# Kernel optimization log

Measured on AMD Instinct MI355X. Metric: run time of the kernel, lower is better.

The kernel has to match this reference:

```python
import jax, jax.numpy as jnp
import numpy as np

N, E, D_IN, D_H, D_OUT, W = 100000, 1600000, 128, 128, 128, 3
HTC_W, TEMP = 0.01, 1.0  # curvature c = 1.0


def _project(x):
    n = jnp.maximum(jnp.linalg.norm(x, axis=-1, keepdims=True), 1e-12)
    return x * jnp.minimum((1.0 - 1e-5) / n, 1.0)


def _artanh(x):
    x = jnp.clip(x, -1.0 + 1e-6, 1.0 - 1e-6)
    return 0.5 * (jnp.log1p(x) - jnp.log1p(-x))


def _expmap0(v):
    n = jnp.maximum(jnp.linalg.norm(v, axis=-1, keepdims=True), 1e-12)
    return _project(jnp.tanh(n) * v / n)


def _logmap0(y):
    y = _project(y)
    n = jnp.maximum(jnp.linalg.norm(y, axis=-1, keepdims=True), 1e-12)
    return _artanh(n) * y / n


def setup_inputs() -> dict:
    key = jax.random.key(0)
    ks = jax.random.split(key, 24)
    x = jax.random.normal(ks[0], (N, D_IN), dtype=jnp.float32)
    edge_index = jax.random.randint(ks[1], (2, E), 0, N)
    t = jax.random.uniform(ks[2], (E,), dtype=jnp.float32)
    prev_hyp = _project(jax.random.normal(ks[3], (N, D_OUT), dtype=jnp.float32) * 0.05)
    lengths = jax.random.randint(ks[4], (N,), 0, W + 1)
    valid_mask = jnp.arange(W)[None, :] < lengths[:, None]  # front-filled deque
    hist_hyp = _project(jax.random.normal(ks[5], (N, W, D_OUT), dtype=jnp.float32) * 0.05)
    hist_hyp = hist_hyp * valid_mask[..., None].astype(jnp.float32)  # padded slots are zero

    def lin(k, dout, din):
        return jax.random.normal(k, (dout, din), dtype=jnp.float32) / np.sqrt(din)

    params = dict(
        w_time=jax.random.normal(ks[6], (D_IN,), dtype=jnp.float32),
        b_time=jnp.zeros((D_IN,), jnp.float32),
        W0_l=lin(ks[7], D_H, D_IN), b0_l=jnp.zeros((D_H,), jnp.float32), W0_r=lin(ks[8], D_H, D_IN),
        W1_l=lin(ks[9], D_OUT, D_H), b1_l=jnp.zeros((D_OUT,), jnp.float32), W1_r=lin(ks[10], D_OUT, D_H),
        W_ih=lin(ks[11], 3 * D_OUT, D_OUT), W_hh=lin(ks[12], 3 * D_OUT, D_OUT),
        b_ih=jnp.zeros((3 * D_OUT,), jnp.float32), b_hh=jnp.zeros((3 * D_OUT,), jnp.float32),
        Wq=lin(ks[13], D_OUT, D_OUT), Wk=lin(ks[14], D_OUT, D_OUT), Wv=lin(ks[15], D_OUT, D_OUT),
    )
    return dict(x=x, edge_index=edge_index, t=t, prev_hyp=prev_hyp,
                hist_hyp=hist_hyp, valid_mask=valid_mask, **params)


def reference(x, edge_index, t, prev_hyp, hist_hyp, valid_mask,
              w_time, b_time, W0_l, b0_l, W0_r, W1_l, b1_l, W1_r,
              W_ih, W_hh, b_ih, b_hh, Wq, Wk, Wv):
    n = x.shape[0]
    src, dst = edge_index[0], edge_index[1]
    ones_e = jnp.ones_like(t)
    # per-node mean event time over incident edges (src and dst both count)
    nt = jax.ops.segment_sum(t, src, n) + jax.ops.segment_sum(t, dst, n)
    cnt = jax.ops.segment_sum(ones_e, src, n) + jax.ops.segment_sum(ones_e, dst, n)
    node_time = nt / jnp.maximum(cnt, 1.0)
    x = x + jnp.cos(node_time[:, None] * w_time[None, :] + b_time[None, :])
    # SAGEConv (mean aggr over incoming edges): out = W_l @ mean_j x_j + b + W_r @ x_i
    deg = jnp.maximum(jax.ops.segment_sum(ones_e, dst, n), 1.0)[:, None]
    agg0 = jax.ops.segment_sum(x[src], dst, n) / deg
    h = jax.nn.relu(agg0 @ W0_l.T + b0_l + x @ W0_r.T)
    agg1 = jax.ops.segment_sum(h[src], dst, n) / deg
    h_now = agg1 @ W1_l.T + b1_l + h @ W1_r.T  # tangent-space current embedding

    prev_tan = _logmap0(prev_hyp)
    # ragged history attention (padded + masked)
    hist_tan = _logmap0(hist_hyp)                       # [N, W, D]
    q = h_now @ Wq.T                                    # [N, D]
    k = hist_tan @ Wk.T                                 # [N, W, D]
    v = hist_tan @ Wv.T
    score = jnp.einsum('nwd,nd->nw', k, q) / (np.sqrt(D_OUT) * max(TEMP, 1e-6))
    has_hist = valid_mask.any(axis=-1, keepdims=True)
    score = jnp.where(valid_mask, score, -jnp.inf)
    score = jnp.where(has_hist, score, 0.0)
    alpha = jax.nn.softmax(score, axis=-1)
    alpha = jnp.where(has_hist, alpha, 0.0)
    ctx = jnp.einsum('nw,nwd->nd', alpha, v)

    # GRUCell(input=h_now, hidden=prev_tan + ctx)
    hidden = prev_tan + ctx
    gi = h_now @ W_ih.T + b_ih
    gh = hidden @ W_hh.T + b_hh
    i_r, i_z, i_n = jnp.split(gi, 3, axis=-1)
    h_r, h_z, h_n = jnp.split(gh, 3, axis=-1)
    r = jax.nn.sigmoid(i_r + h_r)
    z = jax.nn.sigmoid(i_z + h_z)
    nn_ = jnp.tanh(i_n + r * h_n)
    h_tan = (1.0 - z) * nn_ + z * hidden
    h_hyp = _expmap0(h_tan)

    # hyperbolic temporal consistency aux loss (c = 1)
    x_sq = jnp.sum(h_hyp * h_hyp, axis=-1)
    y_sq = jnp.sum(prev_hyp * prev_hyp, axis=-1)
    diff_sq = jnp.sum((h_hyp - prev_hyp) ** 2, axis=-1)
    denom = jnp.maximum((1.0 - x_sq) * (1.0 - y_sq), 1e-8)
    zarg = jnp.maximum(1.0 + 2.0 * diff_sq / denom, 1.0 + 1e-6)
    dist = jnp.arccosh(zarg)
    valid_prev = (jnp.sum(jnp.abs(prev_hyp), axis=-1) > 0).astype(dist.dtype)
    aux = HTC_W * jnp.sum(dist * valid_prev) / jnp.maximum(jnp.sum(valid_prev), 1.0)
    aux = jnp.where(jnp.any(valid_prev > 0), aux, 0.0)
    return h_hyp, aux
```

## Files before the change

kernel.cpp:

```cpp
#include <hip/hip_runtime.h>
#include <math.h>


typedef _Float16 f16x8 __attribute__((ext_vector_type(8)));
typedef _Float16 f16x4 __attribute__((ext_vector_type(4)));
typedef _Float16 f16x2 __attribute__((ext_vector_type(2)));
typedef float f32x4 __attribute__((ext_vector_type(4)));

__device__ __forceinline__ float wsum(float v) {
#pragma unroll
  for (int off = 1; off < 64; off <<= 1) v += __shfl_xor(v, off, 64);
  return v;
}

__device__ __forceinline__ void fsplit(float x, _Float16& h, _Float16& l) {
  h = (_Float16)x;
  l = (_Float16)(x - (float)h);
}

__device__ __forceinline__ float logmap_scale(float nrm2) {
  float n0 = fmaxf(sqrtf(nrm2), 1e-12f);
  float sp = fminf((1.0f - 1e-5f) / n0, 1.0f);
  float np = fmaxf(n0 * sp, 1e-12f);
  float a  = fminf(np, 1.0f - 1e-6f);
  float at = 0.5f * (log1pf(a) - log1pf(-a));
  return sp * at / np;
}

__global__ void k_edge(const int* __restrict__ ei, const float* __restrict__ t,
                       unsigned long long* __restrict__ packed, int E) {
  int e = blockIdx.x * 256 + threadIdx.x;
  if (e >= E) return;
  int s = ei[e], d = ei[E + e];
  unsigned long long tf =
      (unsigned long long)__float2uint_rn(t[e] * 16777216.0f);
  unsigned long long encs = tf | (1ULL << 40);
  atomicAdd(&packed[s], encs);
  atomicAdd(&packed[d], encs | (1ULL << 52));
}

__global__ void k_scan1(const unsigned long long* __restrict__ packed,
                        int* __restrict__ rowptr, int* __restrict__ bsum, int N) {
  __shared__ int s[256];
  int t = threadIdx.x;
  int base = blockIdx.x * 1024 + t * 4;
  int v[4]; int loc = 0;
#pragma unroll
  for (int j = 0; j < 4; ++j) {
    int i = base + j;
    v[j] = (i < N) ? (int)(packed[i] >> 52) : 0;
    loc += v[j];
  }
  s[t] = loc; __syncthreads();
  for (int off = 1; off < 256; off <<= 1) {
    int x = (t >= off) ? s[t - off] : 0; __syncthreads();
    s[t] += x; __syncthreads();
  }
  int run = s[t] - loc;
#pragma unroll
  for (int j = 0; j < 4; ++j) { int i = base + j; if (i < N) rowptr[i] = run; run += v[j]; }
  if (t == 255) bsum[blockIdx.x] = s[255];
}

__global__ void k_scan2(const int* __restrict__ bsum, int* __restrict__ boff, int nb) {
  __shared__ int s[128];
  int t = threadIdx.x;
  int v = (t < nb) ? bsum[t] : 0;
  s[t] = v; __syncthreads();
  for (int off = 1; off < 128; off <<= 1) {
    int x = (t >= off) ? s[t - off] : 0; __syncthreads();
    s[t] += x; __syncthreads();
  }
  boff[t] = s[t] - v;
}

__global__ void k_scan3(int* __restrict__ rowptr, const int* __restrict__ boff, int N, int E) {
  int i = blockIdx.x * 256 + threadIdx.x;
  if (i < N) rowptr[i] += boff[i >> 10];
  if (i == 0) rowptr[N] = E;
}

__global__ void k_scatter(const int* __restrict__ ei, const int* __restrict__ rowptr,
                          int* __restrict__ cursor, int* __restrict__ eidx, int E) {
  int e = blockIdx.x * 256 + threadIdx.x;
  if (e >= E) return;
  int s = ei[e], d = ei[E + e];
  int p = rowptr[d] + atomicAdd(&cursor[d], 1);
  eidx[p] = s;
}

__global__ void k_time(const float* __restrict__ x,
                       const unsigned long long* __restrict__ packed,
                       const float* __restrict__ wt,
                       const float* __restrict__ bt, float* __restrict__ outF,
                       _Float16* __restrict__ outH, _Float16* __restrict__ outL, int N) {
  int id = blockIdx.x * 256 + threadIdx.x;
  if (id >= N * 32) return;
  int n = id >> 5, q = id & 31;
  unsigned long long p = packed[n];
  float tsum = (float)(p & 0xFFFFFFFFFFULL) * 5.9604644775390625e-8f;
  int c = (int)((p >> 40) & 0xFFF);
  float tm = tsum / fmaxf((float)c, 1.0f);
  float4 xv = ((const float4*)x)[id];
  float4 wv = ((const float4*)wt)[q];
  float4 bv = ((const float4*)bt)[q];
  float o[4];
  o[0] = xv.x + cosf(tm * wv.x + bv.x);
  o[1] = xv.y + cosf(tm * wv.y + bv.y);
  o[2] = xv.z + cosf(tm * wv.z + bv.z);
  o[3] = xv.w + cosf(tm * wv.w + bv.w);
  ((float4*)outF)[id] = make_float4(o[0], o[1], o[2], o[3]);
  f16x4 vh, vl;
#pragma unroll
  for (int j = 0; j < 4; ++j) { _Float16 h, l; fsplit(o[j], h, l); vh[j] = h; vl[j] = l; }
  *(f16x4*)&outH[(size_t)id * 4] = vh;
  *(f16x4*)&outL[(size_t)id * 4] = vl;
}

__global__ void k_agg(const float* __restrict__ X, const int* __restrict__ rowptr,
                      const int* __restrict__ eidx, _Float16* __restrict__ outH,
                      _Float16* __restrict__ outL, int N) {
  int wid = threadIdx.x >> 6, lane = threadIdx.x & 63;
  int n = blockIdx.x * 4 + wid;
  if (n >= N) return;
  int s0 = rowptr[n], s1 = rowptr[n + 1];
  float ax = 0.f, ay = 0.f;
  for (int e = s0; e < s1; ++e) {
    int s = eidx[e];
    float2 v = ((const float2*)X)[(size_t)s * 64 + lane];
    ax += v.x; ay += v.y;
  }
  float sc = 1.0f / fmaxf((float)(s1 - s0), 1.0f);
  _Float16 hx, lx, hy, ly;
  fsplit(ax * sc, hx, lx); fsplit(ay * sc, hy, ly);
  f16x2 vh = {hx, hy}, vl = {lx, ly};
  *(f16x2*)&outH[(size_t)n * 128 + lane * 2] = vh;
  *(f16x2*)&outL[(size_t)n * 128 + lane * 2] = vl;
}

__global__ void k_prep(const float* __restrict__ W0l, const float* __restrict__ W0r,
                       const float* __restrict__ W1l, const float* __restrict__ W1r,
                       const float* __restrict__ Wv,  const float* __restrict__ Wih,
                       const float* __restrict__ Whh, const float* __restrict__ bih,
                       const float* __restrict__ bhh,
                       _Float16* __restrict__ W0H, _Float16* __restrict__ W0L,
                       _Float16* __restrict__ W1H, _Float16* __restrict__ W1L,
                       _Float16* __restrict__ WvH, _Float16* __restrict__ WvL,
                       _Float16* __restrict__ WzH, _Float16* __restrict__ WzL,
                       float* __restrict__ bz) {
  int id = blockIdx.x * 256 + threadIdx.x;
  if (id < 32768) {
    int c = id >> 8, k = id & 255;
    float v0 = (k < 128) ? W0l[c * 128 + k] : W0r[c * 128 + (k - 128)];
    float v1 = (k < 128) ? W1l[c * 128 + k] : W1r[c * 128 + (k - 128)];
    fsplit(v0, W0H[id], W0L[id]);
    fsplit(v1, W1H[id], W1L[id]);
  }
  if (id < 16384) {
    fsplit(Wv[id], WvH[id], WvL[id]);
  }
  if (id < 131072) {
    int c = id >> 8, k = id & 255;
    float v;
    if (c < 256)      v = (k < 128) ? Wih[c * 128 + k] : Whh[c * 128 + (k - 128)];
    else if (c < 384) v = (k < 128) ? Wih[c * 128 + k] : 0.f;
    else              v = (k < 128) ? 0.f : Whh[(c - 128) * 128 + (k - 128)];
    fsplit(v, WzH[id], WzL[id]);
  }
  if (id < 512) {
    float v;
    if (id < 256)      v = bih[id] + bhh[id];
    else if (id < 384) v = bih[id];
    else               v = bhh[id - 128];
    bz[id] = v;
  }
}

__global__ void k_ct(const float* __restrict__ Wk, const float* __restrict__ Wq,
                     _Float16* __restrict__ CtH, _Float16* __restrict__ CtL) {
  int id = blockIdx.x * 256 + threadIdx.x;
  if (id >= 16384) return;
  int c = id >> 7, k = id & 127;
  float s = 0.f;
  for (int j = 0; j < 128; ++j) s += Wk[j * 128 + c] * Wq[j * 128 + k];
  fsplit(s, CtH[id], CtL[id]);
}

__global__ __launch_bounds__(256)
void k_mm(const _Float16* __restrict__ A1H, const _Float16* __restrict__ A1L,
          const _Float16* __restrict__ A2H, const _Float16* __restrict__ A2L,
          const _Float16* __restrict__ WH,  const _Float16* __restrict__ WL,
          const float* __restrict__ bias,   const float* __restrict__ addb,
          float* __restrict__ outF, _Float16* __restrict__ outH,
          _Float16* __restrict__ outL,
          int Nrows, int Ktot, int Ctot, int relu) {
  __shared__ _Float16 sA[2][128][64];
  __shared__ _Float16 sW[2][128][64];
  const int tid = threadIdx.x;
  const int lane = tid & 63;
  const int wv = tid >> 6;
  const int wr = wv >> 1, wc = wv & 1;
  const int laneR = lane & 15, laneG = lane >> 4;
  const int n0 = blockIdx.x * 128;
  const int c0 = blockIdx.y * 128;

  f32x4 acc[4][4];
#pragma unroll
  for (int mi = 0; mi < 4; ++mi)
#pragma unroll
    for (int ni = 0; ni < 4; ++ni)
#pragma unroll
      for (int j = 0; j < 4; ++j) acc[mi][ni][j] = 0.f;

  const int nslab = Ktot >> 6;
  for (int s = 0; s < nslab; ++s) {
    int kglob = s << 6;
    const _Float16* aH = (kglob < 128) ? A1H : A2H;
    const _Float16* aL = (kglob < 128) ? A1L : A2L;
    int kc = kglob & 127;
    __syncthreads();
#pragma unroll
    for (int it = 0; it < 4; ++it) {
      int idx = tid + (it << 8);
      int r = idx >> 3, chunk = idx & 7;
      int cs = (chunk ^ (r & 7)) << 3;
      int kq = chunk << 3;
      int n = n0 + r;
      f16x8 vh, vl;
      if (n < Nrows) {
        vh = *(const f16x8*)&aH[(size_t)n * 128 + kc + kq];
        vl = *(const f16x8*)&aL[(size_t)n * 128 + kc + kq];
      } else {
#pragma unroll
        for (int j = 0; j < 8; ++j) { vh[j] = (_Float16)0; vl[j] = (_Float16)0; }
      }
      *(f16x8*)&sA[0][r][cs] = vh;
      *(f16x8*)&sA[1][r][cs] = vl;
      int c = c0 + r;
      f16x8 wh = *(const f16x8*)&WH[(size_t)c * Ktot + kglob + kq];
      f16x8 wl = *(const f16x8*)&WL[(size_t)c * Ktot + kglob + kq];
      *(f16x8*)&sW[0][r][cs] = wh;
      *(f16x8*)&sW[1][r][cs] = wl;
    }
    __syncthreads();
#pragma unroll
    for (int kk = 0; kk < 2; ++kk) {
      f16x8 ah[4], al[4], bh[4], bl[4];
      int kch = (kk << 2) + laneG;
#pragma unroll
      for (int m = 0; m < 4; ++m) {
        int row = wr * 64 + m * 16 + laneR;
        int ko = (kch ^ (row & 7)) << 3;
        ah[m] = *(const f16x8*)&sA[0][row][ko];
        al[m] = *(const f16x8*)&sA[1][row][ko];
      }
#pragma unroll
      for (int n = 0; n < 4; ++n) {
        int row = wc * 64 + n * 16 + laneR;
        int ko = (kch ^ (row & 7)) << 3;
        bh[n] = *(const f16x8*)&sW[0][row][ko];
        bl[n] = *(const f16x8*)&sW[1][row][ko];
      }
#pragma unroll
      for (int m = 0; m < 4; ++m)
#pragma unroll
        for (int n = 0; n < 4; ++n) {
          acc[m][n] = __builtin_amdgcn_mfma_f32_16x16x32_f16(ah[m], bh[n], acc[m][n], 0, 0, 0);
          acc[m][n] = __builtin_amdgcn_mfma_f32_16x16x32_f16(al[m], bh[n], acc[m][n], 0, 0, 0);
          acc[m][n] = __builtin_amdgcn_mfma_f32_16x16x32_f16(ah[m], bl[n], acc[m][n], 0, 0, 0);
        }
    }
  }
#pragma unroll
  for (int m = 0; m < 4; ++m) {
#pragma unroll
    for (int n = 0; n < 4; ++n) {
      int rbase = n0 + wr * 64 + m * 16 + laneG * 4;
      int c = c0 + wc * 64 + n * 16 + laneR;
      float bval = bias ? bias[c] : 0.f;
#pragma unroll
      for (int j = 0; j < 4; ++j) {
        int r = rbase + j;
        if (r >= Nrows) continue;
        float v = acc[m][n][j] + bval;
        if (addb) v += addb[(size_t)r * Ctot + c];
        if (relu) v = fmaxf(v, 0.f);
        if (outF) outF[(size_t)r * Ctot + c] = v;
        if (outH) {
          _Float16 h, l; fsplit(v, h, l);
          outH[(size_t)r * Ctot + c] = h;
          outL[(size_t)r * Ctot + c] = l;
        }
      }
    }
  }
}

__global__ void k_logmap(const float* __restrict__ Y, float* __restrict__ out, int N) {
  int wid = threadIdx.x >> 6, lane = threadIdx.x & 63;
  int n = blockIdx.x * 4 + wid;
  if (n >= N) return;
  float2 y = ((const float2*)Y)[(size_t)n * 64 + lane];
  float nrm2 = wsum(y.x * y.x + y.y * y.y);
  float s = logmap_scale(nrm2);
  ((float2*)out)[(size_t)n * 64 + lane] = make_float2(y.x * s, y.y * s);
}

__global__ void k_attn(const float* __restrict__ U, const float* __restrict__ hist,
                       _Float16* __restrict__ outH, _Float16* __restrict__ outL, int N) {
  int wid = threadIdx.x >> 6, lane = threadIdx.x & 63;
  int n = blockIdx.x * 4 + wid;
  if (n >= N) return;
  float2 u = ((const float2*)U)[(size_t)n * 64 + lane];
  float htx[3], hty[3], sc[3];
  bool val[3];
#pragma unroll
  for (int w = 0; w < 3; ++w) {
    float2 h = ((const float2*)hist)[((size_t)n * 3 + w) * 64 + lane];
    float nrm2 = wsum(h.x * h.x + h.y * h.y);
    val[w] = nrm2 > 0.f;
    float s = logmap_scale(nrm2);
    htx[w] = h.x * s; hty[w] = h.y * s;
    float d = wsum(htx[w] * u.x + hty[w] * u.y);
    sc[w] = d * 0.0883883476483184f;
  }
  float cx = 0.f, cy = 0.f;
  if (val[0] || val[1] || val[2]) {
    float m = -INFINITY;
#pragma unroll
    for (int w = 0; w < 3; ++w) if (val[w]) m = fmaxf(m, sc[w]);
    float a[3]; float ssum = 0.f;
#pragma unroll
    for (int w = 0; w < 3; ++w) { a[w] = val[w] ? expf(sc[w] - m) : 0.f; ssum += a[w]; }
    float inv = 1.f / ssum;
#pragma unroll
    for (int w = 0; w < 3; ++w) { cx += htx[w] * (a[w] * inv); cy += hty[w] * (a[w] * inv); }
  }
  _Float16 hx, lx, hy, ly;
  fsplit(cx, hx, lx); fsplit(cy, hy, ly);
  f16x2 vh = {hx, hy}, vl = {lx, ly};
  *(f16x2*)&outH[(size_t)n * 128 + lane * 2] = vh;
  *(f16x2*)&outL[(size_t)n * 128 + lane * 2] = vl;
}

__global__ void k_final(const float* __restrict__ Z, const float* __restrict__ HID,
                        const float* __restrict__ prev, float* __restrict__ out,
                        float* __restrict__ pd, float* __restrict__ pv, int N) {
  __shared__ float sdist[4], svalid[4];
  int wid = threadIdx.x >> 6, lane = threadIdx.x & 63;
  int n = blockIdx.x * 4 + wid;
  float dsum = 0.f, vsum = 0.f;
  if (n < N) {
    const float2* z2 = (const float2*)(Z + (size_t)n * 512);
    float2 zr = z2[lane], zz = z2[64 + lane], zi = z2[128 + lane], zh = z2[192 + lane];
    float2 hid = ((const float2*)HID)[(size_t)n * 64 + lane];
    float rx = 1.f / (1.f + expf(-zr.x)), ry = 1.f / (1.f + expf(-zr.y));
    float zx = 1.f / (1.f + expf(-zz.x)), zy = 1.f / (1.f + expf(-zz.y));
    float nx = tanhf(zi.x + rx * zh.x),   ny = tanhf(zi.y + ry * zh.y);
    float tx = (1.f - zx) * nx + zx * hid.x;
    float ty = (1.f - zy) * ny + zy * hid.y;
    float nv2 = wsum(tx * tx + ty * ty);
    float nv = fmaxf(sqrtf(nv2), 1e-12f);
    float tn = tanhf(nv);
    float s1 = tn / nv;
    float wx = tx * s1, wy = ty * s1;
    float nw = fmaxf(tn, 1e-12f);
    float sp = fminf((1.f - 1e-5f) / nw, 1.f);
    float hx = wx * sp, hy = wy * sp;
    float2 p = ((const float2*)prev)[(size_t)n * 64 + lane];
    float x_sq = wsum(hx * hx + hy * hy);
    float y_sq = wsum(p.x * p.x + p.y * p.y);
    float dx = hx - p.x, dy = hy - p.y;
    float d_sq = wsum(dx * dx + dy * dy);
    float pab = wsum(fabsf(p.x) + fabsf(p.y));
    float denom = fmaxf((1.f - x_sq) * (1.f - y_sq), 1e-8f);
    float zarg = fmaxf(1.f + 2.f * d_sq / denom, 1.f + 1e-6f);
    float dist = acoshf(zarg);
    float valid = (pab > 0.f) ? 1.f : 0.f;
    dsum = dist * valid; vsum = valid;
    ((float2*)out)[(size_t)n * 64 + lane] = make_float2(hx, hy);
  }
  if (lane == 0) { sdist[wid] = dsum; svalid[wid] = vsum; }
  __syncthreads();
  if (threadIdx.x == 0) {
    pd[blockIdx.x] = sdist[0] + sdist[1] + sdist[2] + sdist[3];
    pv[blockIdx.x] = svalid[0] + svalid[1] + svalid[2] + svalid[3];
  }
}

__global__ void k_reduce(const float* __restrict__ pd, const float* __restrict__ pv,
                         float* __restrict__ aux_out, int nparts) {
  __shared__ float sd[256], sv[256];
  float a = 0.f, b = 0.f;
  for (int i = threadIdx.x; i < nparts; i += 256) { a += pd[i]; b += pv[i]; }
  sd[threadIdx.x] = a; sv[threadIdx.x] = b; __syncthreads();
  for (int off = 128; off > 0; off >>= 1) {
    if (threadIdx.x < off) { sd[threadIdx.x] += sd[threadIdx.x + off]; sv[threadIdx.x] += sv[threadIdx.x + off]; }
    __syncthreads();
  }
  if (threadIdx.x == 0) {
    float aux = (sv[0] > 0.f) ? 0.01f * sd[0] / fmaxf(sv[0], 1.f) : 0.f;
    aux_out[0] = aux;
  }
}

extern "C" void kernel_launch(void* const* d_in, const int* in_sizes, int n_in,
                              void* d_out, int out_size, void* d_ws, size_t ws_size,
                              hipStream_t stream) {
  const float* x      = (const float*)d_in[0];
  const int*   ei     = (const int*)  d_in[1];
  const float* t      = (const float*)d_in[2];
  const float* prev   = (const float*)d_in[3];
  const float* hist   = (const float*)d_in[4];
  const float* w_time = (const float*)d_in[6];
  const float* b_time = (const float*)d_in[7];
  const float* W0l    = (const float*)d_in[8];
  const float* b0l    = (const float*)d_in[9];
  const float* W0r    = (const float*)d_in[10];
  const float* W1l    = (const float*)d_in[11];
  const float* b1l    = (const float*)d_in[12];
  const float* W1r    = (const float*)d_in[13];
  const float* Wih    = (const float*)d_in[14];
  const float* Whh    = (const float*)d_in[15];
  const float* bih    = (const float*)d_in[16];
  const float* bhh    = (const float*)d_in[17];
  const float* Wq     = (const float*)d_in[18];
  const float* Wk     = (const float*)d_in[19];
  const float* Wv     = (const float*)d_in[20];

  const int N = in_sizes[0] / 128;
  const int E = in_sizes[1] / 2;
  const int NB4 = (N + 3) / 4;
  const int NB1 = (N + 1023) / 1024;

  char* wbase = (char*)d_ws;
  size_t off = 0;
  auto alloc = [&](size_t bytes) -> void* {
    off = (off + 255) & ~(size_t)255;
    void* p = wbase + off; off += bytes; return p;
  };
  unsigned long long* packed = (unsigned long long*)alloc((size_t)N * 8);
  int*   cursor = (int*)  alloc((size_t)N * 4);
  size_t zero_bytes = off;
  int*   rowptr = (int*)  alloc((size_t)(N + 1) * 4);
  int*   bsum   = (int*)  alloc(512);
  int*   boff   = (int*)  alloc(512);
  int*   eidx   = (int*)  alloc((size_t)E * 4);
  _Float16* W0H = (_Float16*)alloc(32768 * 2);
  _Float16* W0L = (_Float16*)alloc(32768 * 2);
  _Float16* W1H = (_Float16*)alloc(32768 * 2);
  _Float16* W1L = (_Float16*)alloc(32768 * 2);
  _Float16* CtH = (_Float16*)alloc(16384 * 2);
  _Float16* CtL = (_Float16*)alloc(16384 * 2);
  _Float16* WvH = (_Float16*)alloc(16384 * 2);
  _Float16* WvL = (_Float16*)alloc(16384 * 2);
  _Float16* WzH = (_Float16*)alloc(131072 * 2);
  _Float16* WzL = (_Float16*)alloc(131072 * 2);
  float* bz     = (float*)alloc(512 * 4);
  float* F0 = (float*)alloc((size_t)N * 128 * 4);
  float* F1 = (float*)alloc((size_t)N * 128 * 4);
  float* F4 = (float*)alloc((size_t)N * 128 * 4);
  float* F5 = (float*)alloc((size_t)N * 512 * 4);
  _Float16* P0H = (_Float16*)alloc((size_t)N * 128 * 2);
  _Float16* P0L = (_Float16*)alloc((size_t)N * 128 * 2);
  _Float16* P1H = (_Float16*)alloc((size_t)N * 128 * 2);
  _Float16* P1L = (_Float16*)alloc((size_t)N * 128 * 2);
  _Float16* P2H = (_Float16*)alloc((size_t)N * 128 * 2);
  _Float16* P2L = (_Float16*)alloc((size_t)N * 128 * 2);
  float* pd = (float*)alloc((size_t)NB4 * 4);
  float* pv = (float*)alloc((size_t)NB4 * 4);
  (void)ws_size; (void)n_in; (void)out_size;

  float* out_h   = (float*)d_out;
  float* out_aux = out_h + (size_t)N * 128;

  hipMemsetAsync(d_ws, 0, zero_bytes, stream);

  k_prep<<<512, 256, 0, stream>>>(W0l, W0r, W1l, W1r, Wv, Wih, Whh, bih, bhh,
                                  W0H, W0L, W1H, W1L, WvH, WvL, WzH, WzL, bz);
  k_ct<<<64, 256, 0, stream>>>(Wk, Wq, CtH, CtL);

  int ebl = (E + 255) / 256;
  k_edge<<<ebl, 256, 0, stream>>>(ei, t, packed, E);
  k_scan1<<<NB1, 256, 0, stream>>>(packed, rowptr, bsum, N);
  k_scan2<<<1, 128, 0, stream>>>(bsum, boff, NB1);
  k_scan3<<<(N + 255) / 256, 256, 0, stream>>>(rowptr, boff, N, E);
  k_scatter<<<ebl, 256, 0, stream>>>(ei, rowptr, cursor, eidx, E);

  k_time<<<(N * 32 + 255) / 256, 256, 0, stream>>>(x, packed, w_time, b_time,
                                                   F0, P0H, P0L, N);
  k_agg<<<NB4, 256, 0, stream>>>(F0, rowptr, eidx, P1H, P1L, N);
  dim3 gb((N + 127) / 128, 1), gz((N + 127) / 128, 4);
  k_mm<<<gb, 256, 0, stream>>>(P1H, P1L, P0H, P0L, W0H, W0L, b0l, nullptr,
                               F1, P2H, P2L, N, 256, 128, 1);
  k_agg<<<NB4, 256, 0, stream>>>(F1, rowptr, eidx, P1H, P1L, N);
  k_mm<<<gb, 256, 0, stream>>>(P1H, P1L, P2H, P2L, W1H, W1L, b1l, nullptr,
                               nullptr, P0H, P0L, N, 256, 128, 0);
  k_mm<<<gb, 256, 0, stream>>>(P0H, P0L, nullptr, nullptr, CtH, CtL, nullptr, nullptr,
                               F0, nullptr, nullptr, N, 128, 128, 0);
  k_attn<<<NB4, 256, 0, stream>>>(F0, hist, P1H, P1L, N);
  k_logmap<<<NB4, 256, 0, stream>>>(prev, F1, N);
  k_mm<<<gb, 256, 0, stream>>>(P1H, P1L, nullptr, nullptr, WvH, WvL, nullptr, F1,
                               F4, P2H, P2L, N, 128, 128, 0);
  k_mm<<<gz, 256, 0, stream>>>(P0H, P0L, P2H, P2L, WzH, WzL, bz, nullptr,
                               F5, nullptr, nullptr, N, 256, 512, 0);
  k_final<<<NB4, 256, 0, stream>>>(F5, F4, prev, out_h, pd, pv, N);
  k_reduce<<<1, 256, 0, stream>>>(pd, pv, out_aux, NB4);
}
```

Measured before the change: 1.302 ms.

## Fuse GRU gate GEMM with GRU, expmap and aux-loss epilogue into one kernel

Replaces the 512-wide gate GEMM (which wrote an N×512 fp32 gate buffer) and the separate k_final pass with a single k_gru kernel. It computes all four gate blocks per 64-row tile in registers and applies the GRU, expmap0 projection and hyperbolic distance partial sums in the epilogue. The hidden state is reconstructed from the split-fp16 P2 buffers instead of a separate fp32 F4 copy. This removes large intermediate global writes and reads, at the cost of heavy register use (64 accumulators per thread) and reloading weight tiles per K step with less parallelism.

Result: faster. 1.213 ms (-6.8%).

```diff
diff --git a/kernel.cpp b/kernel.cpp
--- a/kernel.cpp
+++ b/kernel.cpp
@@ -296,6 +296,224 @@
   }
 }
 
+__global__ __launch_bounds__(256, 2)
+void k_gru(const _Float16* __restrict__ P0H, const _Float16* __restrict__ P0L,
+           const _Float16* __restrict__ P2H, const _Float16* __restrict__ P2L,
+           const _Float16* __restrict__ WzH, const _Float16* __restrict__ WzL,
+           const float* __restrict__ bz, const float* __restrict__ prev,
+           float* __restrict__ out, float* __restrict__ pd,
+           float* __restrict__ pv, int N) {
+  __shared__ _Float16 sA[2][64][64];
+  __shared__ _Float16 sW[2][128][64];
+  __shared__ float rn1[64][2];
+  __shared__ float rn3[64][2][3];
+  __shared__ float distrow[64], validrow[64];
+  const int tid = threadIdx.x;
+  const int lane = tid & 63;
+  const int wv = tid >> 6;
+  const int wr = wv >> 1, wc = wv & 1;
+  const int laneR = lane & 15, laneG = lane >> 4;
+  const int n0 = blockIdx.x * 64;
+
+  f32x4 acc[4][2][4];
+#pragma unroll
+  for (int q = 0; q < 4; ++q)
+#pragma unroll
+    for (int m = 0; m < 2; ++m)
+#pragma unroll
+      for (int n = 0; n < 4; ++n)
+#pragma unroll
+        for (int j = 0; j < 4; ++j) acc[q][m][n][j] = 0.f;
+
+#pragma unroll
+  for (int s = 0; s < 4; ++s) {
+    int kglob = s << 6;
+    const _Float16* aH = (kglob < 128) ? P0H : P2H;
+    const _Float16* aL = (kglob < 128) ? P0L : P2L;
+    int kc = kglob & 127;
+    __syncthreads();
+#pragma unroll
+    for (int it = 0; it < 2; ++it) {
+      int idx = tid + (it << 8);
+      int r = idx >> 3, chunk = idx & 7;
+      int cs = (chunk ^ (r & 7)) << 3;
+      int kq = chunk << 3;
+      int n = n0 + r;
+      f16x8 vh, vl;
+      if (n < N) {
+        vh = *(const f16x8*)&aH[(size_t)n * 128 + kc + kq];
+        vl = *(const f16x8*)&aL[(size_t)n * 128 + kc + kq];
+      } else {
+#pragma unroll
+        for (int j = 0; j < 8; ++j) { vh[j] = (_Float16)0; vl[j] = (_Float16)0; }
+      }
+      *(f16x8*)&sA[0][r][cs] = vh;
+      *(f16x8*)&sA[1][r][cs] = vl;
+    }
+#pragma unroll
+    for (int q = 0; q < 4; ++q) {
+      if (q) __syncthreads();
+#pragma unroll
+      for (int it = 0; it < 4; ++it) {
+        int idx = tid + (it << 8);
+        int r = idx >> 3, chunk = idx & 7;
+        int cs = (chunk ^ (r & 7)) << 3;
+        int kq = chunk << 3;
+        size_t wrow = (size_t)(q * 128 + r);
+        *(f16x8*)&sW[0][r][cs] = *(const f16x8*)&WzH[wrow * 256 + kglob + kq];
+        *(f16x8*)&sW[1][r][cs] = *(const f16x8*)&WzL[wrow * 256 + kglob + kq];
+      }
+      __syncthreads();
+#pragma unroll
+      for (int kk = 0; kk < 2; ++kk) {
+        int kch = (kk << 2) + laneG;
+        f16x8 ah[2], al[2], bh[4], bl[4];
+#pragma unroll
+        for (int m = 0; m < 2; ++m) {
+          int row = wr * 32 + m * 16 + laneR;
+          int ko = (kch ^ (row & 7)) << 3;
+          ah[m] = *(const f16x8*)&sA[0][row][ko];
+          al[m] = *(const f16x8*)&sA[1][row][ko];
+        }
+#pragma unroll
+        for (int n = 0; n < 4; ++n) {
+          int row = wc * 64 + n * 16 + laneR;
+          int ko = (kch ^ (row & 7)) << 3;
+          bh[n] = *(const f16x8*)&sW[0][row][ko];
+          bl[n] = *(const f16x8*)&sW[1][row][ko];
+        }
+#pragma unroll
+        for (int m = 0; m < 2; ++m)
+#pragma unroll
+          for (int n = 0; n < 4; ++n) {
+            acc[q][m][n] = __builtin_amdgcn_mfma_f32_16x16x32_f16(ah[m], bh[n], acc[q][m][n], 0, 0, 0);
+            acc[q][m][n] = __builtin_amdgcn_mfma_f32_16x16x32_f16(al[m], bh[n], acc[q][m][n], 0, 0, 0);
+            acc[q][m][n] = __builtin_amdgcn_mfma_f32_16x16x32_f16(ah[m], bl[n], acc[q][m][n], 0, 0, 0);
+          }
+      }
+    }
+  }
+
+  float bz0[4], bz1[4], bz2[4], bz3[4];
+#pragma unroll
+  for (int n = 0; n < 4; ++n) {
+    int d = wc * 64 + n * 16 + laneR;
+    bz0[n] = bz[d]; bz1[n] = bz[128 + d]; bz2[n] = bz[256 + d]; bz3[n] = bz[384 + d];
+  }
+  float tv[2][4][4];
+#pragma unroll
+  for (int m = 0; m < 2; ++m)
+#pragma unroll
+    for (int n = 0; n < 4; ++n)
+#pragma unroll
+      for (int j = 0; j < 4; ++j) {
+        int row = n0 + wr * 32 + m * 16 + laneG * 4 + j;
+        int d = wc * 64 + n * 16 + laneR;
+        float hid = 0.f;
+        if (row < N) {
+          size_t o = (size_t)row * 128 + d;
+          hid = (float)P2H[o] + (float)P2L[o];
+        }
+        float gr = acc[0][m][n][j] + bz0[n];
+        float gz = acc[1][m][n][j] + bz1[n];
+        float gi = acc[2][m][n][j] + bz2[n];
+        float gh = acc[3][m][n][j] + bz3[n];
+        float rr = 1.f / (1.f + expf(-gr));
+        float zz = 1.f / (1.f + expf(-gz));
+        float nn = tanhf(gi + rr * gh);
+        tv[m][n][j] = (1.f - zz) * nn + zz * hid;
+      }
+#pragma unroll
+  for (int m = 0; m < 2; ++m)
+#pragma unroll
+    for (int j = 0; j < 4; ++j) {
+      float p = 0.f;
+#pragma unroll
+      for (int n = 0; n < 4; ++n) p += tv[m][n][j] * tv[m][n][j];
+#pragma unroll
+      for (int off = 1; off < 16; off <<= 1) p += __shfl_xor(p, off, 64);
+      if (laneR == 0) rn1[wr * 32 + m * 16 + laneG * 4 + j][wc] = p;
+    }
+  __syncthreads();
+  float hv[2][4][4];
+#pragma unroll
+  for (int m = 0; m < 2; ++m)
+#pragma unroll
+    for (int j = 0; j < 4; ++j) {
+      int rl = wr * 32 + m * 16 + laneG * 4 + j;
+      int row = n0 + rl;
+      float nv2 = rn1[rl][0] + rn1[rl][1];
+      float nv = fmaxf(sqrtf(nv2), 1e-12f);
+      float tn = tanhf(nv);
+      float s1 = tn / nv;
+      float nw = fmaxf(tn, 1e-12f);
+      float sp = fminf((1.f - 1e-5f) / nw, 1.f);
+      float scl = s1 * sp;
+#pragma unroll
+      for (int n = 0; n < 4; ++n) {
+        float h = tv[m][n][j] * scl;
+        hv[m][n][j] = h;
+        int d = wc * 64 + n * 16 + laneR;
+        if (row < N) out[(size_t)row * 128 + d] = h;
+      }
+    }
+#pragma unroll
+  for (int m = 0; m < 2; ++m)
+#pragma unroll
+    for (int j = 0; j < 4; ++j) {
+      int rl = wr * 32 + m * 16 + laneG * 4 + j;
+      int row = n0 + rl;
+      float ys = 0.f, ds = 0.f, pa = 0.f;
+#pragma unroll
+      for (int n = 0; n < 4; ++n) {
+        int d = wc * 64 + n * 16 + laneR;
+        float p = (row < N) ? prev[(size_t)row * 128 + d] : 0.f;
+        float h = hv[m][n][j];
+        ys += p * p; ds += (h - p) * (h - p); pa += fabsf(p);
+      }
+#pragma unroll
+      for (int off = 1; off < 16; off <<= 1) {
+        ys += __shfl_xor(ys, off, 64);
+        ds += __shfl_xor(ds, off, 64);
+        pa += __shfl_xor(pa, off, 64);
+      }
+      if (laneR == 0) { rn3[rl][wc][0] = ys; rn3[rl][wc][1] = ds; rn3[rl][wc][2] = pa; }
+    }
+  __syncthreads();
+  if (wc == 0 && laneR == 0) {
+#pragma unroll
+    for (int m = 0; m < 2; ++m)
+#pragma unroll
+      for (int j = 0; j < 4; ++j) {
+        int rl = wr * 32 + m * 16 + laneG * 4 + j;
+        int row = n0 + rl;
+        float nv2 = rn1[rl][0] + rn1[rl][1];
+        float nv = fmaxf(sqrtf(nv2), 1e-12f);
+        float tn = tanhf(nv);
+        float s1 = tn / nv;
+        float nw = fmaxf(tn, 1e-12f);
+        float sp = fminf((1.f - 1e-5f) / nw, 1.f);
+        float scl = s1 * sp;
+        float x_sq = scl * scl * nv2;
+        float y_sq = rn3[rl][0][0] + rn3[rl][1][0];
+        float d_sq = rn3[rl][0][1] + rn3[rl][1][1];
+        float pab  = rn3[rl][0][2] + rn3[rl][1][2];
+        float denom = fmaxf((1.f - x_sq) * (1.f - y_sq), 1e-8f);
+        float zarg = fmaxf(1.f + 2.f * d_sq / denom, 1.f + 1e-6f);
+        float dist = acoshf(zarg);
+        float valid = (pab > 0.f && row < N) ? 1.f : 0.f;
+        distrow[rl] = dist * valid;
+        validrow[rl] = valid;
+      }
+  }
+  __syncthreads();
+  if (tid < 64) {
+    float dv = distrow[tid], vvv = validrow[tid];
+    dv = wsum(dv); vvv = wsum(vvv);
+    if (tid == 0) { pd[blockIdx.x] = dv; pv[blockIdx.x] = vvv; }
+  }
+}
+
 __global__ void k_logmap(const float* __restrict__ Y, float* __restrict__ out, int N) {
   int wid = threadIdx.x >> 6, lane = threadIdx.x & 63;
   int n = blockIdx.x * 4 + wid;
@@ -341,51 +559,6 @@
   f16x2 vh = {hx, hy}, vl = {lx, ly};
   *(f16x2*)&outH[(size_t)n * 128 + lane * 2] = vh;
   *(f16x2*)&outL[(size_t)n * 128 + lane * 2] = vl;
-}
-
-__global__ void k_final(const float* __restrict__ Z, const float* __restrict__ HID,
-                        const float* __restrict__ prev, float* __restrict__ out,
-                        float* __restrict__ pd, float* __restrict__ pv, int N) {
-  __shared__ float sdist[4], svalid[4];
-  int wid = threadIdx.x >> 6, lane = threadIdx.x & 63;
-  int n = blockIdx.x * 4 + wid;
-  float dsum = 0.f, vsum = 0.f;
-  if (n < N) {
-    const float2* z2 = (const float2*)(Z + (size_t)n * 512);
-    float2 zr = z2[lane], zz = z2[64 + lane], zi = z2[128 + lane], zh = z2[192 + lane];
-    float2 hid = ((const float2*)HID)[(size_t)n * 64 + lane];
-    float rx = 1.f / (1.f + expf(-zr.x)), ry = 1.f / (1.f + expf(-zr.y));
-    float zx = 1.f / (1.f + expf(-zz.x)), zy = 1.f / (1.f + expf(-zz.y));
-    float nx = tanhf(zi.x + rx * zh.x),   ny = tanhf(zi.y + ry * zh.y);
-    float tx = (1.f - zx) * nx + zx * hid.x;
-    float ty = (1.f - zy) * ny + zy * hid.y;
-    float nv2 = wsum(tx * tx + ty * ty);
-    float nv = fmaxf(sqrtf(nv2), 1e-12f);
-    float tn = tanhf(nv);
-    float s1 = tn / nv;
-    float wx = tx * s1, wy = ty * s1;
-    float nw = fmaxf(tn, 1e-12f);
-    float sp = fminf((1.f - 1e-5f) / nw, 1.f);
-    float hx = wx * sp, hy = wy * sp;
-    float2 p = ((const float2*)prev)[(size_t)n * 64 + lane];
-    float x_sq = wsum(hx * hx + hy * hy);
-    float y_sq = wsum(p.x * p.x + p.y * p.y);
-    float dx = hx - p.x, dy = hy - p.y;
-    float d_sq = wsum(dx * dx + dy * dy);
-    float pab = wsum(fabsf(p.x) + fabsf(p.y));
-    float denom = fmaxf((1.f - x_sq) * (1.f - y_sq), 1e-8f);
-    float zarg = fmaxf(1.f + 2.f * d_sq / denom, 1.f + 1e-6f);
-    float dist = acoshf(zarg);
-    float valid = (pab > 0.f) ? 1.f : 0.f;
-    dsum = dist * valid; vsum = valid;
-    ((float2*)out)[(size_t)n * 64 + lane] = make_float2(hx, hy);
-  }
-  if (lane == 0) { sdist[wid] = dsum; svalid[wid] = vsum; }
-  __syncthreads();
-  if (threadIdx.x == 0) {
-    pd[blockIdx.x] = sdist[0] + sdist[1] + sdist[2] + sdist[3];
-    pv[blockIdx.x] = svalid[0] + svalid[1] + svalid[2] + svalid[3];
-  }
 }
 
 __global__ void k_reduce(const float* __restrict__ pd, const float* __restrict__ pv,
@@ -432,6 +605,7 @@
   const int E = in_sizes[1] / 2;
   const int NB4 = (N + 3) / 4;
   const int NB1 = (N + 1023) / 1024;
+  const int NBG = (N + 63) / 64;
 
   char* wbase = (char*)d_ws;
   size_t off = 0;
@@ -459,16 +633,14 @@
   float* bz     = (float*)alloc(512 * 4);
   float* F0 = (float*)alloc((size_t)N * 128 * 4);
   float* F1 = (float*)alloc((size_t)N * 128 * 4);
-  float* F4 = (float*)alloc((size_t)N * 128 * 4);
-  float* F5 = (float*)alloc((size_t)N * 512 * 4);
   _Float16* P0H = (_Float16*)alloc((size_t)N * 128 * 2);
   _Float16* P0L = (_Float16*)alloc((size_t)N * 128 * 2);
   _Float16* P1H = (_Float16*)alloc((size_t)N * 128 * 2);
   _Float16* P1L = (_Float16*)alloc((size_t)N * 128 * 2);
   _Float16* P2H = (_Float16*)alloc((size_t)N * 128 * 2);
   _Float16* P2L = (_Float16*)alloc((size_t)N * 128 * 2);
-  float* pd = (float*)alloc((size_t)NB4 * 4);
-  float* pv = (float*)alloc((size_t)NB4 * 4);
+  float* pd = (float*)alloc((size_t)NBG * 4);
+  float* pv = (float*)alloc((size_t)NBG * 4);
   (void)ws_size; (void)n_in; (void)out_size;
 
   float* out_h   = (float*)d_out;
@@ -490,7 +662,7 @@
   k_time<<<(N * 32 + 255) / 256, 256, 0, stream>>>(x, packed, w_time, b_time,
                                                    F0, P0H, P0L, N);
   k_agg<<<NB4, 256, 0, stream>>>(F0, rowptr, eidx, P1H, P1L, N);
-  dim3 gb((N + 127) / 128, 1), gz((N + 127) / 128, 4);
+  dim3 gb((N + 127) / 128, 1);
   k_mm<<<gb, 256, 0, stream>>>(P1H, P1L, P0H, P0L, W0H, W0L, b0l, nullptr,
                                F1, P2H, P2L, N, 256, 128, 1);
   k_agg<<<NB4, 256, 0, stream>>>(F1, rowptr, eidx, P1H, P1L, N);
@@ -501,9 +673,8 @@
   k_attn<<<NB4, 256, 0, stream>>>(F0, hist, P1H, P1L, N);
   k_logmap<<<NB4, 256, 0, stream>>>(prev, F1, N);
   k_mm<<<gb, 256, 0, stream>>>(P1H, P1L, nullptr, nullptr, WvH, WvL, nullptr, F1,
-                               F4, P2H, P2L, N, 128, 128, 0);
-  k_mm<<<gz, 256, 0, stream>>>(P0H, P0L, P2H, P2L, WzH, WzL, bz, nullptr,
-                               F5, nullptr, nullptr, N, 256, 512, 0);
-  k_final<<<NB4, 256, 0, stream>>>(F5, F4, prev, out_h, pd, pv, N);
-  k_reduce<<<1, 256, 0, stream>>>(pd, pv, out_aux, NB4);
-}
+                               nullptr, P2H, P2L, N, 128, 128, 0);
+  k_gru<<<NBG, 256, 0, stream>>>(P0H, P0L, P2H, P2L, WzH, WzL, bz, prev,
+                                 out_h, pd, pv, N);
+  k_reduce<<<1, 256, 0, stream>>>(pd, pv, out_aux, NBG);
+}
```
